# Kernel tuning notes

Hardware: AMD Instinct MI355X
Metric: run time of the kernel (lower is better)

## Reference

```python
import jax, jax.numpy as jnp
import numpy as np

D_MODEL, N_LEVELS, N_HEADS, N_POINTS = 256, 4, 8, 4
SHAPES = [(100, 100), (50, 50), (25, 25), (13, 13)]  # (H, W) per level


def setup_inputs() -> dict:
    key = jax.random.key(0)
    ks = jax.random.split(key, 8)
    N = 2
    C = D_MODEL
    Len_in = sum(h * w for h, w in SHAPES)
    Lq = Len_in  # encoder self-attention
    query = jax.random.normal(ks[0], (N, Lq, C), jnp.float32)
    reference_points = jax.random.uniform(ks[1], (N, Lq, N_LEVELS, 2), dtype=jnp.float32)
    input_flatten = jax.random.normal(ks[2], (N, Len_in, C), jnp.float32)
    input_spatial_shapes = np.array(SHAPES, dtype=np.int64)
    areas = input_spatial_shapes[:, 0] * input_spatial_shapes[:, 1]
    input_level_start_index = np.concatenate([[0], np.cumsum(areas)[:-1]]).astype(np.int64)
    s = 1.0 / np.sqrt(C)
    Wv = jax.random.uniform(ks[3], (C, C), jnp.float32, -s, s)
    bv = jnp.zeros((C,), jnp.float32)
    # sampling_offsets: small random weight + the module's grid bias init
    Woff = jax.random.normal(ks[4], (N_HEADS * N_LEVELS * N_POINTS * 2, C), jnp.float32) * 0.01
    thetas = jnp.arange(N_HEADS, dtype=jnp.float32) * (2.0 * np.pi / N_HEADS)
    grid = jnp.stack([jnp.cos(thetas), jnp.sin(thetas)], -1)  # (M,2)
    grid = grid / jnp.max(jnp.abs(grid), axis=-1, keepdims=True)
    grid = jnp.tile(grid[:, None, None, :], (1, N_LEVELS, N_POINTS, 1))
    grid = grid * (jnp.arange(N_POINTS, dtype=jnp.float32) + 1.0)[None, None, :, None]
    boff = grid.reshape(-1)
    Wa = jax.random.normal(ks[5], (N_HEADS * N_LEVELS * N_POINTS, C), jnp.float32) * 0.02
    ba = jnp.zeros((N_HEADS * N_LEVELS * N_POINTS,), jnp.float32)
    Wo = jax.random.uniform(ks[6], (C, C), jnp.float32, -s, s)
    bo = jnp.zeros((C,), jnp.float32)
    return {
        'query': query, 'reference_points': reference_points, 'input_flatten': input_flatten,
        'input_spatial_shapes': input_spatial_shapes, 'input_level_start_index': input_level_start_index,
        'Wv': Wv, 'bv': bv, 'Woff': Woff, 'boff': boff, 'Wa': Wa, 'ba': ba, 'Wo': Wo, 'bo': bo,
    }


def _msda_forward(query, reference_points, input_flatten, shapes, starts,
                  Wv, bv, Woff, boff, Wa, ba, Wo, bo):
    N, Lq, C = query.shape
    M, L, P = N_HEADS, N_LEVELS, N_POINTS
    D = C // M
    value = (input_flatten @ Wv.T + bv).reshape(N, -1, M, D)  # (N, Len_in, M, D)
    off = (query @ Woff.T + boff).reshape(N, Lq, M, L, P, 2)
    attn = jax.nn.softmax((query @ Wa.T + ba).reshape(N, Lq, M, L * P), axis=-1)
    attn = attn.reshape(N, Lq, M, L, P)
    # offset_normalizer = (W_l, H_l)
    norm = jnp.asarray(shapes[:, ::-1].copy(), jnp.float32)  # (L, 2)
    loc = reference_points[:, :, None, :, None, :] + off / norm[None, None, None, :, None, :]
    grids = 2.0 * loc - 1.0  # (N, Lq, M, L, P, 2), grid_sample convention
    out = jnp.zeros((N, Lq, M, D), query.dtype)
    for l in range(L):
        H, W = int(shapes[l, 0]), int(shapes[l, 1])
        s0 = int(starts[l])
        v = value[:, s0:s0 + H * W]  # (N, H*W, M, D)
        # align_corners=False unnormalization
        gx = ((grids[:, :, :, l, :, 0] + 1.0) * W - 1.0) / 2.0  # (N, Lq, M, P)
        gy = ((grids[:, :, :, l, :, 1] + 1.0) * H - 1.0) / 2.0
        x0 = jnp.floor(gx); y0 = jnp.floor(gy)
        fx = gx - x0;       fy = gy - y0
        x0i = x0.astype(jnp.int32); y0i = y0.astype(jnp.int32)

        def gather(iy, ix):
            valid = (iy >= 0) & (iy < H) & (ix >= 0) & (ix < W)
            lin = jnp.clip(iy, 0, H - 1) * W + jnp.clip(ix, 0, W - 1)  # (N, Lq, M, P)
            lin2 = lin.transpose(0, 1, 3, 2).reshape(N, Lq * P, M)
            g = jnp.take_along_axis(v, lin2[..., None], axis=1)  # (N, Lq*P, M, D)
            g = g.reshape(N, Lq, P, M, D).transpose(0, 1, 3, 2, 4)  # (N, Lq, M, P, D)
            return g * valid[..., None]  # zero padding outside

        s00 = gather(y0i, x0i)
        s01 = gather(y0i, x0i + 1)
        s10 = gather(y0i + 1, x0i)
        s11 = gather(y0i + 1, x0i + 1)
        sampled = (s00 * ((1 - fy) * (1 - fx))[..., None] + s01 * ((1 - fy) * fx)[..., None]
                   + s10 * (fy * (1 - fx))[..., None] + s11 * (fy * fx)[..., None])
        out = out + jnp.einsum('nqmp,nqmpd->nqmd', attn[:, :, :, l], sampled)
    out = out.reshape(N, Lq, C)
    return out @ Wo.T + bo


def reference(query, reference_points, input_flatten, input_spatial_shapes, input_level_start_index,
              Wv, bv, Woff, boff, Wa, ba, Wo, bo):
    shapes = np.asarray(input_spatial_shapes)
    starts = np.asarray(input_level_start_index)
    return _msda_forward(query, reference_points, input_flatten, shapes, starts,
                         Wv, bv, Woff, boff, Wa, ba, Wo, bo)
```

## Files before the change

kernel.cpp:

```cpp
#include <hip/hip_runtime.h>
#include <math.h>

#define NB   2
#define LQ   13294
#define NROWS (NB*LQ)
#define CDIM 256

typedef unsigned short u16;
typedef unsigned int   u32;
typedef short bf16x8 __attribute__((ext_vector_type(8)));
typedef float f32x4  __attribute__((ext_vector_type(4)));

struct alignas(8) U16x4 { u16 x, y, z, w; };

__device__ __forceinline__ u16 f2bf(float f) {
    u32 u = __builtin_bit_cast(u32, f);
    u += 0x7FFFu + ((u >> 16) & 1u);
    return (u16)(u >> 16);
}
__device__ __forceinline__ float bf2f(u16 h) {
    u32 u = ((u32)h) << 16;
    return __builtin_bit_cast(float, u);
}

__global__ __launch_bounds__(256)
void prep_all(const float4* __restrict__ query, const float4* __restrict__ inflat,
              const float* __restrict__ Wv, const float* __restrict__ Woff,
              const float* __restrict__ Wa, const float* __restrict__ Wo,
              const float* __restrict__ boff, const float* __restrict__ ba,
              u16* __restrict__ qb, u16* __restrict__ ib,
              u16* __restrict__ wb, float* __restrict__ biascat) {
    const int b = blockIdx.x;
    const int t = threadIdx.x;
    if (b < 6647) {
        int i = b * 256 + t;
        float4 v = query[i];
        U16x4 o{f2bf(v.x), f2bf(v.y), f2bf(v.z), f2bf(v.w)};
        *(U16x4*)&qb[(size_t)i * 4] = o;
    } else if (b < 13294) {
        int i = (b - 6647) * 256 + t;
        float4 v = inflat[i];
        U16x4 o{f2bf(v.x), f2bf(v.y), f2bf(v.z), f2bf(v.w)};
        *(U16x4*)&ib[(size_t)i * 4] = o;
    } else {
        int i = (b - 13294) * 256 + t;
        float v;
        if      (i <  65536) v = Wv[i];
        else if (i < 131072) v = Woff[i - 65536];
        else if (i < 163840) v = Wa[i - 131072];
        else                 v = Wo[i - 163840];
        wb[i] = f2bf(v);
        if (b == 13294) {
            biascat[t] = boff[t];
            if (t < 128) biascat[256 + t] = ba[t];
        }
    }
}

template<int MODE>
__global__ __launch_bounds__(64, 2)
void gemm_breg(const u16* __restrict__ A, const u16* __restrict__ Bw,
               const float* __restrict__ bias, void* __restrict__ C0,
               float* __restrict__ C1, int M) {
    const int lane = threadIdx.x;
    const int ln16 = lane & 15;
    const int kq   = lane >> 4;
    const int col0 = blockIdx.x * 64;
    const int rt0  = blockIdx.y * 64;

    bf16x8 b[4][8];
    #pragma unroll
    for (int j = 0; j < 4; ++j) {
        const u16* Bp = Bw + (size_t)(col0 + j * 16 + ln16) * 256 + kq * 8;
        #pragma unroll
        for (int kt = 0; kt < 8; ++kt)
            b[j][kt] = *(const bf16x8*)(Bp + kt * 32);
    }
    float bs[4];
    #pragma unroll
    for (int j = 0; j < 4; ++j) bs[j] = bias[col0 + j * 16 + ln16];

    bf16x8 a[2][8];
    {
        int gr = min(rt0 + ln16, M - 1);
        const u16* Ap = A + (size_t)gr * 256 + kq * 8;
        #pragma unroll
        for (int kt = 0; kt < 8; ++kt) a[0][kt] = *(const bf16x8*)(Ap + kt * 32);
    }
    #pragma unroll
    for (int rt = 0; rt < 4; ++rt) {
        if (rt < 3) {
            int gr = min(rt0 + (rt + 1) * 16 + ln16, M - 1);
            const u16* Ap = A + (size_t)gr * 256 + kq * 8;
            #pragma unroll
            for (int kt = 0; kt < 8; ++kt)
                a[(rt + 1) & 1][kt] = *(const bf16x8*)(Ap + kt * 32);
        }
        f32x4 acc[4] = {};
        #pragma unroll
        for (int kt = 0; kt < 8; ++kt)
            #pragma unroll
            for (int j = 0; j < 4; ++j)
                acc[j] = __builtin_amdgcn_mfma_f32_16x16x32_bf16(
                    a[rt & 1][kt], b[j][kt], acc[j], 0, 0, 0);

        #pragma unroll
        for (int j = 0; j < 4; ++j) {
            int gc = col0 + j * 16 + ln16;
            #pragma unroll
            for (int r = 0; r < 4; ++r) {
                int gr = rt0 + rt * 16 + kq * 4 + r;
                if (gr < M) {
                    float o = acc[j][r] + bs[j];
                    if (MODE == 0)
                        ((u16*)C0)[(size_t)gr * 256 + gc] = f2bf(o);
                    else if (MODE == 2)
                        ((float*)C0)[(size_t)gr * 256 + gc] = o;
                    else {
                        if (gc < 256) ((float*)C0)[(size_t)gr * 256 + gc] = o;
                        else          C1[(size_t)gr * 128 + (gc - 256)] = o;
                    }
                }
            }
        }
    }
}

__global__ __launch_bounds__(256)
void msda_sample(const u16* __restrict__ value,
                 const float* __restrict__ refpts,
                 const float* __restrict__ off,
                 const float* __restrict__ logits,
                 u16* __restrict__ tmp) {
    __shared__ float sAw[4][8][16];
    __shared__ int   sLin[4][8][17][4];
    __shared__ float sW[4][8][17][4];

    const int t  = threadIdx.x;
    const int qb = blockIdx.x * 4;

    if (t < 32) {
        const int qi = t >> 3, m = t & 7;
        const float* lg = logits + (size_t)(qb + qi) * 128 + m * 16;
        float e[16];
        float mx = -1e30f;
        #pragma unroll
        for (int i = 0; i < 16; ++i) { e[i] = lg[i]; mx = fmaxf(mx, e[i]); }
        float s = 0.f;
        #pragma unroll
        for (int i = 0; i < 16; ++i) { e[i] = __expf(e[i] - mx); s += e[i]; }
        const float inv = 1.f / s;
        #pragma unroll
        for (int i = 0; i < 16; ++i) sAw[qi][m][i] = e[i] * inv;
    }
    __syncthreads();

    #pragma unroll
    for (int j2 = 0; j2 < 2; ++j2) {
        const int job = t + j2 * 256;
        const int qi = job >> 7;
        const int m  = (job >> 4) & 7;
        const int p  = job & 15;
        const int l  = p >> 2, pp = p & 3;
        const int q  = qb + qi;
        const int n  = (q >= LQ) ? 1 : 0;

        const int W = (l == 0) ? 100 : (l == 1) ? 50 : (l == 2) ? 25 : 13;
        const int H = W;
        const int st = (l == 0) ? 0 : (l == 1) ? 10000 : (l == 2) ? 12500 : 13125;

        const float rx = refpts[(size_t)q * 8 + l * 2 + 0];
        const float ry = refpts[(size_t)q * 8 + l * 2 + 1];
        const float ox = off[(size_t)q * 256 + m * 32 + (l * 4 + pp) * 2 + 0];
        const float oy = off[(size_t)q * 256 + m * 32 + (l * 4 + pp) * 2 + 1];

        const float locx = rx + ox / (float)W;
        const float locy = ry + oy / (float)H;
        const float grx = 2.f * locx - 1.f;
        const float gry = 2.f * locy - 1.f;
        const float gx = ((grx + 1.f) * (float)W - 1.f) * 0.5f;
        const float gy = ((gry + 1.f) * (float)H - 1.f) * 0.5f;
        const float x0f = floorf(gx), y0f = floorf(gy);
        const float fx = gx - x0f, fy = gy - y0f;
        const int x0 = (int)x0f, y0 = (int)y0f;
        const int x1 = x0 + 1, y1 = y0 + 1;

        const int cx0 = min(max(x0, 0), W - 1);
        const int cx1 = min(max(x1, 0), W - 1);
        const int cy0 = min(max(y0, 0), H - 1);
        const int cy1 = min(max(y1, 0), H - 1);
        const bool vx0 = (x0 >= 0) & (x0 < W);
        const bool vx1 = (x1 >= 0) & (x1 < W);
        const bool vy0 = (y0 >= 0) & (y0 < H);
        const bool vy1 = (y1 >= 0) & (y1 < H);

        const float aw = sAw[qi][m][p];
        const int base = n * LQ + st;
        sLin[qi][m][p][0] = base + cy0 * W + cx0;
        sLin[qi][m][p][1] = base + cy0 * W + cx1;
        sLin[qi][m][p][2] = base + cy1 * W + cx0;
        sLin[qi][m][p][3] = base + cy1 * W + cx1;
        sW[qi][m][p][0] = (vy0 & vx0) ? aw * (1.f - fy) * (1.f - fx) : 0.f;
        sW[qi][m][p][1] = (vy0 & vx1) ? aw * (1.f - fy) * fx         : 0.f;
        sW[qi][m][p][2] = (vy1 & vx0) ? aw * fy * (1.f - fx)         : 0.f;
        sW[qi][m][p][3] = (vy1 & vx1) ? aw * fy * fx                 : 0.f;
    }
    __syncthreads();

    const int qi = t >> 6;
    const int m  = (t >> 3) & 7;
    const int e  = t & 7;
    const int q  = qb + qi;
    const u16* vch = value + m * 32 + e * 4;

    float ax = 0.f, ay = 0.f, az = 0.f, aw_ = 0.f;
    #pragma unroll
    for (int g = 0; g < 4; ++g) {
        U16x4 raw[16];
        float4 Wt4[4];
        #pragma unroll
        for (int pp = 0; pp < 4; ++pp) {
            int p = g * 4 + pp;
            int4 L = *(const int4*)&sLin[qi][m][p][0];
            Wt4[pp] = *(const float4*)&sW[qi][m][p][0];
            raw[pp * 4 + 0] = *(const U16x4*)(vch + (size_t)L.x * 256);
            raw[pp * 4 + 1] = *(const U16x4*)(vch + (size_t)L.y * 256);
            raw[pp * 4 + 2] = *(const U16x4*)(vch + (size_t)L.z * 256);
            raw[pp * 4 + 3] = *(const U16x4*)(vch + (size_t)L.w * 256);
        }
        #pragma unroll
        for (int pp = 0; pp < 4; ++pp) {
            const float* wp = (const float*)&Wt4[pp];
            #pragma unroll
            for (int c = 0; c < 4; ++c) {
                U16x4 r = raw[pp * 4 + c];
                float wgt = wp[c];
                ax  += wgt * bf2f(r.x);
                ay  += wgt * bf2f(r.y);
                az  += wgt * bf2f(r.z);
                aw_ += wgt * bf2f(r.w);
            }
        }
    }
    U16x4 o{f2bf(ax), f2bf(ay), f2bf(az), f2bf(aw_)};
    *(U16x4*)&tmp[(size_t)q * 256 + m * 32 + e * 4] = o;
}

extern "C" void kernel_launch(void* const* d_in, const int* in_sizes, int n_in,
                              void* d_out, int out_size, void* d_ws, size_t ws_size,
                              hipStream_t stream) {
    const float* query  = (const float*)d_in[0];
    const float* refpts = (const float*)d_in[1];
    const float* inflat = (const float*)d_in[2];
    const float* Wv   = (const float*)d_in[5];
    const float* bv   = (const float*)d_in[6];
    const float* Woff = (const float*)d_in[7];
    const float* boff = (const float*)d_in[8];
    const float* Wa   = (const float*)d_in[9];
    const float* ba   = (const float*)d_in[10];
    const float* Wo   = (const float*)d_in[11];
    const float* bo   = (const float*)d_in[12];
    float* out = (float*)d_out;

    char* ws = (char*)d_ws;
    constexpr size_t SZ16 = (size_t)NROWS * 256 * 2;
    constexpr size_t SZ32 = (size_t)NROWS * 256 * 4;
    constexpr size_t SZL  = (size_t)NROWS * 128 * 4;
    u16*   qb    = (u16*)(ws);
    u16*   ib    = (u16*)(ws + SZ16);
    u16*   value = (u16*)(ws + 2 * SZ16);
    float* offb  = (float*)(ws + 3 * SZ16);
    float* logit = (float*)(ws + 3 * SZ16 + SZ32);
    u16*   wb    = (u16*)(ws + 3 * SZ16 + SZ32 + SZL);
    float* bcat  = (float*)(ws + 3 * SZ16 + SZ32 + SZL + 229376 * 2);
    u16*   tmp   = qb;

    const int RG = (NROWS + 63) / 64;

    hipLaunchKernelGGL(prep_all, dim3(14190), dim3(256), 0, stream,
                       (const float4*)query, (const float4*)inflat,
                       Wv, Woff, Wa, Wo, boff, ba, qb, ib, wb, bcat);

    gemm_breg<0><<<dim3(4, RG), dim3(64), 0, stream>>>(
        ib, wb, bv, (void*)value, nullptr, NROWS);
    gemm_breg<1><<<dim3(6, RG), dim3(64), 0, stream>>>(
        qb, wb + 65536, bcat, (void*)offb, logit, NROWS);

    hipLaunchKernelGGL(msda_sample, dim3(NROWS / 4), dim3(256), 0, stream,
                       value, refpts, offb, logit, tmp);

    gemm_breg<2><<<dim3(4, RG), dim3(64), 0, stream>>>(
        tmp, wb + 163840, bo, (void*)out, nullptr, NROWS);
}
```

Before: 245.8 us.

## Replace register-B GEMMs with LDS-tiled 4-wave GEMM and merge front projections

Replaces the single-wave GEMM, which holds B in registers, with a 256-thread kernel. It stages 64x64 A and B tiles through swizzled shared memory across four K steps, and each wave computes a 32x32 sub-tile. The value projection and the offset/logit projection are merged into one launch with 10 column blocks. The intent is better occupancy and global load coalescing, plus one fewer launch. The cost is extra LDS traffic and two barriers per K step.

```diff
diff --git a/kernel.cpp b/kernel.cpp
--- a/kernel.cpp
+++ b/kernel.cpp
@@ -57,70 +57,125 @@
     }
 }
 
-template<int MODE>
-__global__ __launch_bounds__(64, 2)
-void gemm_breg(const u16* __restrict__ A, const u16* __restrict__ Bw,
-               const float* __restrict__ bias, void* __restrict__ C0,
-               float* __restrict__ C1, int M) {
-    const int lane = threadIdx.x;
+__device__ __forceinline__ void gemm_core64(
+    const u16* __restrict__ A, const u16* __restrict__ Bw, int M, int row0,
+    u16* As, u16* Bs, f32x4 (&acc)[2][2]) {
+    const int tid  = threadIdx.x;
+    const int wave = tid >> 6;
+    const int lane = tid & 63;
     const int ln16 = lane & 15;
     const int kq   = lane >> 4;
-    const int col0 = blockIdx.x * 64;
-    const int rt0  = blockIdx.y * 64;
-
-    bf16x8 b[4][8];
-    #pragma unroll
-    for (int j = 0; j < 4; ++j) {
-        const u16* Bp = Bw + (size_t)(col0 + j * 16 + ln16) * 256 + kq * 8;
-        #pragma unroll
-        for (int kt = 0; kt < 8; ++kt)
-            b[j][kt] = *(const bf16x8*)(Bp + kt * 32);
-    }
-    float bs[4];
-    #pragma unroll
-    for (int j = 0; j < 4; ++j) bs[j] = bias[col0 + j * 16 + ln16];
-
-    bf16x8 a[2][8];
-    {
-        int gr = min(rt0 + ln16, M - 1);
-        const u16* Ap = A + (size_t)gr * 256 + kq * 8;
-        #pragma unroll
-        for (int kt = 0; kt < 8; ++kt) a[0][kt] = *(const bf16x8*)(Ap + kt * 32);
-    }
-    #pragma unroll
-    for (int rt = 0; rt < 4; ++rt) {
-        if (rt < 3) {
-            int gr = min(rt0 + (rt + 1) * 16 + ln16, M - 1);
-            const u16* Ap = A + (size_t)gr * 256 + kq * 8;
-            #pragma unroll
-            for (int kt = 0; kt < 8; ++kt)
-                a[(rt + 1) & 1][kt] = *(const bf16x8*)(Ap + kt * 32);
-        }
-        f32x4 acc[4] = {};
-        #pragma unroll
-        for (int kt = 0; kt < 8; ++kt)
-            #pragma unroll
-            for (int j = 0; j < 4; ++j)
-                acc[j] = __builtin_amdgcn_mfma_f32_16x16x32_bf16(
-                    a[rt & 1][kt], b[j][kt], acc[j], 0, 0, 0);
-
-        #pragma unroll
-        for (int j = 0; j < 4; ++j) {
-            int gc = col0 + j * 16 + ln16;
+    const int wrow = (wave >> 1) * 32;
+    const int wcol = (wave & 1) * 32;
+
+    #pragma unroll
+    for (int kt = 0; kt < 4; ++kt) {
+        const int k0 = kt * 64;
+        #pragma unroll
+        for (int it = 0; it < 2; ++it) {
+            int chunk = it * 256 + tid;
+            int row = chunk >> 3;
+            int ch  = chunk & 7;
+            int gra = min(row0 + row, M - 1);
+            float4 va = *(const float4*)(A  + (size_t)gra * 256 + k0 + ch * 8);
+            float4 vb = *(const float4*)(Bw + (size_t)row * 256 + k0 + ch * 8);
+            *(float4*)&As[row * 64 + (ch ^ (row & 7)) * 8] = va;
+            *(float4*)&Bs[row * 64 + (ch ^ (row & 7)) * 8] = vb;
+        }
+        __syncthreads();
+        #pragma unroll
+        for (int kf = 0; kf < 2; ++kf) {
+            int ck = kf * 4 + kq;
+            bf16x8 a[2], b[2];
+            #pragma unroll
+            for (int i = 0; i < 2; ++i) {
+                int r = wrow + i * 16 + ln16;
+                a[i] = *(const bf16x8*)&As[r * 64 + ((ck ^ (r & 7)) * 8)];
+                int c = wcol + i * 16 + ln16;
+                b[i] = *(const bf16x8*)&Bs[c * 64 + ((ck ^ (c & 7)) * 8)];
+            }
+            #pragma unroll
+            for (int i = 0; i < 2; ++i)
+                #pragma unroll
+                for (int j = 0; j < 2; ++j)
+                    acc[i][j] = __builtin_amdgcn_mfma_f32_16x16x32_bf16(
+                        a[i], b[j], acc[i][j], 0, 0, 0);
+        }
+        __syncthreads();
+    }
+}
+
+__global__ __launch_bounds__(256, 4)
+void gemm_front(const u16* __restrict__ qb, const u16* __restrict__ ib,
+                const u16* __restrict__ wb, const float* __restrict__ bv,
+                const float* __restrict__ bcat, u16* __restrict__ value,
+                float* __restrict__ offb, float* __restrict__ logit, int M) {
+    __shared__ u16 As[64 * 64];
+    __shared__ u16 Bs[64 * 64];
+    const int s    = blockIdx.x;
+    const int row0 = blockIdx.y * 64;
+    const u16* A  = (s < 4) ? ib : qb;
+    const u16* Bw = (s < 4) ? wb + (size_t)s * 64 * 256
+                            : wb + 65536 + (size_t)(s - 4) * 64 * 256;
+    const float* bias = (s < 4) ? bv + s * 64 : bcat + (s - 4) * 64;
+
+    f32x4 acc[2][2] = {};
+    gemm_core64(A, Bw, M, row0, As, Bs, acc);
+
+    const int lane = threadIdx.x & 63;
+    const int wave = threadIdx.x >> 6;
+    const int ln16 = lane & 15, kq = lane >> 4;
+    const int wrow = (wave >> 1) * 32, wcol = (wave & 1) * 32;
+    #pragma unroll
+    for (int j = 0; j < 2; ++j) {
+        int lc = wcol + j * 16 + ln16;
+        float bj = bias[lc];
+        #pragma unroll
+        for (int i = 0; i < 2; ++i) {
             #pragma unroll
             for (int r = 0; r < 4; ++r) {
-                int gr = rt0 + rt * 16 + kq * 4 + r;
+                int gr = row0 + wrow + i * 16 + kq * 4 + r;
                 if (gr < M) {
-                    float o = acc[j][r] + bs[j];
-                    if (MODE == 0)
-                        ((u16*)C0)[(size_t)gr * 256 + gc] = f2bf(o);
-                    else if (MODE == 2)
-                        ((float*)C0)[(size_t)gr * 256 + gc] = o;
+                    float o = acc[i][j][r] + bj;
+                    if (s < 4)
+                        value[(size_t)gr * 256 + s * 64 + lc] = f2bf(o);
                     else {
-                        if (gc < 256) ((float*)C0)[(size_t)gr * 256 + gc] = o;
-                        else          C1[(size_t)gr * 128 + (gc - 256)] = o;
+                        int gc = (s - 4) * 64 + lc;
+                        if (gc < 256) offb[(size_t)gr * 256 + gc] = o;
+                        else          logit[(size_t)gr * 128 + (gc - 256)] = o;
                     }
                 }
+            }
+        }
+    }
+}
+
+__global__ __launch_bounds__(256, 4)
+void gemm_out(const u16* __restrict__ A, const u16* __restrict__ Bw0,
+              const float* __restrict__ bias, float* __restrict__ C, int M) {
+    __shared__ u16 As[64 * 64];
+    __shared__ u16 Bs[64 * 64];
+    const int s    = blockIdx.x;
+    const int row0 = blockIdx.y * 64;
+    const u16* Bw = Bw0 + (size_t)s * 64 * 256;
+
+    f32x4 acc[2][2] = {};
+    gemm_core64(A, Bw, M, row0, As, Bs, acc);
+
+    const int lane = threadIdx.x & 63;
+    const int wave = threadIdx.x >> 6;
+    const int ln16 = lane & 15, kq = lane >> 4;
+    const int wrow = (wave >> 1) * 32, wcol = (wave & 1) * 32;
+    #pragma unroll
+    for (int j = 0; j < 2; ++j) {
+        int gc = s * 64 + wcol + j * 16 + ln16;
+        float bj = bias[gc];
+        #pragma unroll
+        for (int i = 0; i < 2; ++i) {
+            #pragma unroll
+            for (int r = 0; r < 4; ++r) {
+                int gr = row0 + wrow + i * 16 + kq * 4 + r;
+                if (gr < M) C[(size_t)gr * 256 + gc] = acc[i][j][r] + bj;
             }
         }
     }
@@ -281,14 +336,12 @@
                        (const float4*)query, (const float4*)inflat,
                        Wv, Woff, Wa, Wo, boff, ba, qb, ib, wb, bcat);
 
-    gemm_breg<0><<<dim3(4, RG), dim3(64), 0, stream>>>(
-        ib, wb, bv, (void*)value, nullptr, NROWS);
-    gemm_breg<1><<<dim3(6, RG), dim3(64), 0, stream>>>(
-        qb, wb + 65536, bcat, (void*)offb, logit, NROWS);
+    gemm_front<<<dim3(10, RG), dim3(256), 0, stream>>>(
+        qb, ib, wb, bv, bcat, value, offb, logit, NROWS);
 
     hipLaunchKernelGGL(msda_sample, dim3(NROWS / 4), dim3(256), 0, stream,
                        value, refpts, offb, logit, tmp);
 
-    gemm_breg<2><<<dim3(4, RG), dim3(64), 0, stream>>>(
-        tmp, wb + 163840, bo, (void*)out, nullptr, NROWS);
-}
+    gemm_out<<<dim3(4, RG), dim3(256), 0, stream>>>(
+        tmp, wb + 163840, bo, out, NROWS);
+}
```

Measured after the change: 228.8 us. -6.9%, faster.
